# Kernel tuning notes

Measured on AMD Instinct MI355X. Metric: run time of the kernel, lower is better.

## Reference

```python
import jax, jax.numpy as jnp
import numpy as np

N_E = 1024
E_DIM = 64
BETA = 0.25


def setup_inputs() -> dict:
    key = jax.random.key(0)
    k1, k2 = jax.random.split(key)
    z = jax.random.normal(k1, (32, 32, 32, E_DIM), dtype=jnp.float32)
    # torch init: uniform(-1/n_e, 1/n_e)
    codebook = jax.random.uniform(k2, (N_E, E_DIM), dtype=jnp.float32,
                                  minval=-1.0 / N_E, maxval=1.0 / N_E)
    return {"z": z, "codebook": codebook}


def reference(z, codebook):
    z_flat = z.reshape(-1, E_DIM)  # [N, e_dim]
    # squared euclidean distances: ||z||^2 + ||e||^2 - 2 z e^T
    d = (jnp.sum(z_flat ** 2, axis=1, keepdims=True)
         + jnp.sum(codebook ** 2, axis=1)
         - 2.0 * jnp.matmul(z_flat, codebook.T))  # [N, n_e]
    idx = jnp.argmin(d, axis=1)  # [N]
    z_q = codebook[idx].reshape(z.shape)
    sg = jax.lax.stop_gradient
    loss = jnp.mean((sg(z_q) - z) ** 2) + BETA * jnp.mean((z_q - sg(z)) ** 2)
    z_q_st = z + sg(z_q - z)  # straight-through estimator
    return z_q_st, idx, loss
```

## Files before the change

### kernel.cpp

```cpp
#include <hip/hip_runtime.h>

#define NROWS 32768
#define NE    1024
#define ED    64
#define CHUNK 128
#define NCH   (NE / CHUNK)
#define RPW   8

typedef float4 f4;
typedef float2 f2;

__global__ void vq_prep(const float* __restrict__ cb, float* __restrict__ ssq)
{
    int j = blockIdx.x * blockDim.x + threadIdx.x;
    const f4* crow = (const f4*)(cb + (size_t)j * ED);
    float v[ED];
#pragma unroll
    for (int i = 0; i < 16; ++i) {
        f4 t = crow[i];
        v[4*i+0] = t.x; v[4*i+1] = t.y; v[4*i+2] = t.z; v[4*i+3] = t.w;
    }
    {
#pragma clang fp contract(off)
        float r0 = v[0]*v[0], r1 = v[1]*v[1], r2 = v[2]*v[2], r3 = v[3]*v[3];
        float r4 = v[4]*v[4], r5 = v[5]*v[5], r6 = v[6]*v[6], r7 = v[7]*v[7];
#pragma unroll
        for (int i = 8; i < ED; i += 8) {
            r0 += v[i+0]*v[i+0]; r1 += v[i+1]*v[i+1];
            r2 += v[i+2]*v[i+2]; r3 += v[i+3]*v[i+3];
            r4 += v[i+4]*v[i+4]; r5 += v[i+5]*v[i+5];
            r6 += v[i+6]*v[i+6]; r7 += v[i+7]*v[i+7];
        }
        ssq[j] = ((r0+r1)+(r2+r3)) + ((r4+r5)+(r6+r7));
    }
}

__global__ __launch_bounds__(256, 4)
void vq_main(const float* __restrict__ z, const float* __restrict__ cb,
             const float* __restrict__ ssq, float* __restrict__ out,
             float* __restrict__ partials)
{
    __shared__ __align__(16) float et[ED * CHUNK];
    __shared__ __align__(16) float sqsh[NE];
    __shared__ int   idxsh[32];
    __shared__ float wsum[4];

    const int tid  = threadIdx.x;
    const int lane = tid & 63;
    const int w    = tid >> 6;
    const int w_u  = __builtin_amdgcn_readfirstlane(w);
    const int rowbase = blockIdx.x * 32;

    ((f4*)sqsh)[tid] = ((const f4*)ssq)[tid];

    float cn[RPW];
    {
        const int rl = lane >> 3;
        const int jj = lane & 7;
        const float* zr = z + (size_t)(rowbase + w_u * RPW + rl) * ED;
        float a;
        {
#pragma clang fp contract(off)
            a = 0.f;
#pragma unroll
            for (int i = 0; i < 8; ++i) { float v = zr[8*i + jj]; a += v*v; }
        }
        a += __shfl_xor(a, 1);
        a += __shfl_xor(a, 2);
        a += __shfl_xor(a, 4);
#pragma unroll
        for (int r = 0; r < RPW; ++r) cn[r] = __shfl(a, r * 8);
    }

    float bestv[RPW];
    int   besti[RPW];
#pragma unroll
    for (int r = 0; r < RPW; ++r) { bestv[r] = INFINITY; besti[r] = 0; }

    const f2* et2 = (const f2*)et;
    const float* zw = z + (size_t)(rowbase + w_u * RPW) * ED;

    for (int ch = 0; ch < NCH; ++ch) {
        __syncthreads();
        {
            const int c = tid & 127;
            const int h = tid >> 7;
            const f4* crow = (const f4*)(cb + (size_t)(ch * CHUNK + c) * ED
                                         + h * 32);
#pragma unroll
            for (int i = 0; i < 8; ++i) {
                f4 t = crow[i];
                const int dim = h * 32 + 4 * i;
                et[(dim+0) * CHUNK + c] = t.x;
                et[(dim+1) * CHUNK + c] = t.y;
                et[(dim+2) * CHUNK + c] = t.z;
                et[(dim+3) * CHUNK + c] = t.w;
            }
        }
        __syncthreads();

        f2 sv = ((const f2*)sqsh)[ch * 64 + lane];
        float svq[2] = {sv.x, sv.y};

        float acc[RPW][2];
#pragma unroll
        for (int r = 0; r < RPW; ++r) acc[r][0] = acc[r][1] = 0.f;

#pragma unroll 2
        for (int k4 = 0; k4 < 16; ++k4) {
            f2 e0 = et2[(4*k4+0) * 64 + lane];
            f2 e1 = et2[(4*k4+1) * 64 + lane];
            f2 e2 = et2[(4*k4+2) * 64 + lane];
            f2 e3 = et2[(4*k4+3) * 64 + lane];
            f4 z0 = *(const f4*)(zw + 0*ED + 4*k4);
            f4 z1 = *(const f4*)(zw + 1*ED + 4*k4);
            f4 z2 = *(const f4*)(zw + 2*ED + 4*k4);
            f4 z3 = *(const f4*)(zw + 3*ED + 4*k4);
            f4 z4 = *(const f4*)(zw + 4*ED + 4*k4);
            f4 z5 = *(const f4*)(zw + 5*ED + 4*k4);
            f4 z6 = *(const f4*)(zw + 6*ED + 4*k4);
            f4 z7 = *(const f4*)(zw + 7*ED + 4*k4);
#define ROWFMA(r, zz)                                                    \
            acc[r][0] = fmaf(zz.x, e0.x, acc[r][0]);                     \
            acc[r][1] = fmaf(zz.x, e0.y, acc[r][1]);                     \
            acc[r][0] = fmaf(zz.y, e1.x, acc[r][0]);                     \
            acc[r][1] = fmaf(zz.y, e1.y, acc[r][1]);                     \
            acc[r][0] = fmaf(zz.z, e2.x, acc[r][0]);                     \
            acc[r][1] = fmaf(zz.z, e2.y, acc[r][1]);                     \
            acc[r][0] = fmaf(zz.w, e3.x, acc[r][0]);                     \
            acc[r][1] = fmaf(zz.w, e3.y, acc[r][1]);
            ROWFMA(0, z0) ROWFMA(1, z1) ROWFMA(2, z2) ROWFMA(3, z3)
            ROWFMA(4, z4) ROWFMA(5, z5) ROWFMA(6, z6) ROWFMA(7, z7)
#undef ROWFMA
        }

        {
#pragma clang fp contract(off)
#pragma unroll
            for (int r = 0; r < RPW; ++r) {
#pragma unroll
                for (int q = 0; q < 2; ++q) {
                    float t1 = cn[r] + svq[q];
                    float d  = t1 - 2.0f * acc[r][q];
                    int j = ch * CHUNK + lane * 2 + q;
                    if (d < bestv[r]) { bestv[r] = d; besti[r] = j; }
                }
            }
        }
    }

    float lp = 0.f;
#pragma unroll
    for (int r = 0; r < RPW; ++r) {
        float v = bestv[r];
        int   i = besti[r];
#pragma unroll
        for (int m = 1; m < 64; m <<= 1) {
            float ov = __shfl_xor(v, m);
            int   oi = __shfl_xor(i, m);
            if (ov < v || (ov == v && oi < i)) { v = ov; i = oi; }
        }
        i &= (NE - 1);
        const int grow = rowbase + w * RPW + r;
        float zq, zz, diff, st;
        {
#pragma clang fp contract(off)
            zq   = cb[(size_t)i * ED + lane];
            zz   = z [(size_t)grow * ED + lane];
            diff = zq - zz;
            st   = zz + diff;
            lp  += diff * diff;
        }
        out[(size_t)grow * ED + lane] = st;
        if (lane == 0) idxsh[w * RPW + r] = i;
    }

#pragma unroll
    for (int m = 1; m < 64; m <<= 1) lp += __shfl_xor(lp, m);
    if (lane == 0) wsum[w] = lp;
    __syncthreads();

    if (tid < 32) {
        int iv = idxsh[tid] & (NE - 1);
        out[(size_t)NROWS * ED + rowbase + tid] = (float)iv;
    }
    if (tid == 0)
        partials[blockIdx.x] = (wsum[0] + wsum[1]) + (wsum[2] + wsum[3]);
}

__global__ void vq_finalize(const float* __restrict__ partials,
                            float* __restrict__ out)
{
    __shared__ float red[256];
    int t = threadIdx.x;
    float s = (partials[t] + partials[t + 256]) + (partials[t + 512] + partials[t + 768]);
    red[t] = s;
    __syncthreads();
    for (int m = 128; m > 0; m >>= 1) {
        if (t < m) red[t] += red[t + m];
        __syncthreads();
    }
    if (t == 0) {
        float mean = red[0] / (float)((size_t)NROWS * ED);
        out[(size_t)NROWS * ED + NROWS] = mean + 0.25f * mean;
    }
}

extern "C" void kernel_launch(void* const* d_in, const int* in_sizes, int n_in,
                              void* d_out, int out_size, void* d_ws, size_t ws_size,
                              hipStream_t stream)
{
    (void)in_sizes; (void)n_in; (void)out_size; (void)ws_size;
    const float* z  = (const float*)d_in[0];
    const float* cb = (const float*)d_in[1];
    float* out = (float*)d_out;
    float* ssq      = (float*)d_ws;
    float* partials = ssq + NE;

    vq_prep<<<4, 256, 0, stream>>>(cb, ssq);
    vq_main<<<1024, 256, 0, stream>>>(z, cb, ssq, out, partials);
    vq_finalize<<<1, 256, 0, stream>>>(partials, out);
}
```

Before: 74.38 us.

## Pre-interleave codebook in global memory and split codebook across waves per row group

The prep kernel now also writes a dim-quad-major interleaved copy of the codebook to workspace. The main kernel reads codebook entries directly from global/L2 instead of staging transposed chunks through LDS with per-chunk barriers. Each block now handles 16 rows, with two waves splitting the 1024 codes per 8-row group and merging their argmins through shared memory. The grid is doubled, occupancy is raised to 8 blocks per SIMD, and the epilogue is vectorized to float4. This removes LDS transposes and syncs but relies on L2/cache bandwidth for the codebook reads.

```diff
diff --git a/kernel.cpp b/kernel.cpp
--- a/kernel.cpp
+++ b/kernel.cpp
@@ -3,61 +3,61 @@
 #define NROWS 32768
 #define NE    1024
 #define ED    64
-#define CHUNK 128
-#define NCH   (NE / CHUNK)
-#define RPW   8
 
 typedef float4 f4;
-typedef float2 f2;
-
-__global__ void vq_prep(const float* __restrict__ cb, float* __restrict__ ssq)
+
+__global__ void vq_prep(const float* __restrict__ cb, f4* __restrict__ eTi,
+                        float* __restrict__ ssq)
 {
     int j = blockIdx.x * blockDim.x + threadIdx.x;
     const f4* crow = (const f4*)(cb + (size_t)j * ED);
-    float v[ED];
-#pragma unroll
-    for (int i = 0; i < 16; ++i) {
-        f4 t = crow[i];
-        v[4*i+0] = t.x; v[4*i+1] = t.y; v[4*i+2] = t.z; v[4*i+3] = t.w;
-    }
+    f4 v[16];
+#pragma unroll
+    for (int i = 0; i < 16; ++i) v[i] = crow[i];
     {
 #pragma clang fp contract(off)
-        float r0 = v[0]*v[0], r1 = v[1]*v[1], r2 = v[2]*v[2], r3 = v[3]*v[3];
-        float r4 = v[4]*v[4], r5 = v[5]*v[5], r6 = v[6]*v[6], r7 = v[7]*v[7];
-#pragma unroll
-        for (int i = 8; i < ED; i += 8) {
-            r0 += v[i+0]*v[i+0]; r1 += v[i+1]*v[i+1];
-            r2 += v[i+2]*v[i+2]; r3 += v[i+3]*v[i+3];
-            r4 += v[i+4]*v[i+4]; r5 += v[i+5]*v[i+5];
-            r6 += v[i+6]*v[i+6]; r7 += v[i+7]*v[i+7];
+        float r0 = v[0].x*v[0].x, r1 = v[0].y*v[0].y;
+        float r2 = v[0].z*v[0].z, r3 = v[0].w*v[0].w;
+        float r4 = v[1].x*v[1].x, r5 = v[1].y*v[1].y;
+        float r6 = v[1].z*v[1].z, r7 = v[1].w*v[1].w;
+#pragma unroll
+        for (int q = 2; q < 16; q += 2) {
+            r0 += v[q].x*v[q].x;   r1 += v[q].y*v[q].y;
+            r2 += v[q].z*v[q].z;   r3 += v[q].w*v[q].w;
+            r4 += v[q+1].x*v[q+1].x; r5 += v[q+1].y*v[q+1].y;
+            r6 += v[q+1].z*v[q+1].z; r7 += v[q+1].w*v[q+1].w;
         }
         ssq[j] = ((r0+r1)+(r2+r3)) + ((r4+r5)+(r6+r7));
     }
-}
-
-__global__ __launch_bounds__(256, 4)
+#pragma unroll
+    for (int k4 = 0; k4 < 16; ++k4) eTi[(size_t)k4 * NE + j] = v[k4];
+}
+
+__global__ __launch_bounds__(256, 8)
 void vq_main(const float* __restrict__ z, const float* __restrict__ cb,
-             const float* __restrict__ ssq, float* __restrict__ out,
-             float* __restrict__ partials)
-{
-    __shared__ __align__(16) float et[ED * CHUNK];
-    __shared__ __align__(16) float sqsh[NE];
-    __shared__ int   idxsh[32];
-    __shared__ float wsum[4];
+             const f4* __restrict__ eTi, const float* __restrict__ ssq,
+             float* __restrict__ out, float* __restrict__ partials)
+{
+    __shared__ float cvsh[4][8];
+    __shared__ int   cish[4][8];
+    __shared__ int   idxsh[16];
+    __shared__ float redsh[4];
 
     const int tid  = threadIdx.x;
     const int lane = tid & 63;
     const int w    = tid >> 6;
     const int w_u  = __builtin_amdgcn_readfirstlane(w);
-    const int rowbase = blockIdx.x * 32;
-
-    ((f4*)sqsh)[tid] = ((const f4*)ssq)[tid];
-
-    float cn[RPW];
+    const int rg   = w_u >> 1;
+    const int half = w_u & 1;
+    const int rowbase = blockIdx.x * 16;
+
+    const float* zw = z + (size_t)(rowbase + rg * 8) * ED;
+
+    float cn[8];
     {
         const int rl = lane >> 3;
         const int jj = lane & 7;
-        const float* zr = z + (size_t)(rowbase + w_u * RPW + rl) * ED;
+        const float* zr = zw + (size_t)rl * ED;
         float a;
         {
 #pragma clang fp contract(off)
@@ -69,49 +69,26 @@
         a += __shfl_xor(a, 2);
         a += __shfl_xor(a, 4);
 #pragma unroll
-        for (int r = 0; r < RPW; ++r) cn[r] = __shfl(a, r * 8);
-    }
-
-    float bestv[RPW];
-    int   besti[RPW];
-#pragma unroll
-    for (int r = 0; r < RPW; ++r) { bestv[r] = INFINITY; besti[r] = 0; }
-
-    const f2* et2 = (const f2*)et;
-    const float* zw = z + (size_t)(rowbase + w_u * RPW) * ED;
-
-    for (int ch = 0; ch < NCH; ++ch) {
-        __syncthreads();
-        {
-            const int c = tid & 127;
-            const int h = tid >> 7;
-            const f4* crow = (const f4*)(cb + (size_t)(ch * CHUNK + c) * ED
-                                         + h * 32);
-#pragma unroll
-            for (int i = 0; i < 8; ++i) {
-                f4 t = crow[i];
-                const int dim = h * 32 + 4 * i;
-                et[(dim+0) * CHUNK + c] = t.x;
-                et[(dim+1) * CHUNK + c] = t.y;
-                et[(dim+2) * CHUNK + c] = t.z;
-                et[(dim+3) * CHUNK + c] = t.w;
-            }
-        }
-        __syncthreads();
-
-        f2 sv = ((const f2*)sqsh)[ch * 64 + lane];
-        float svq[2] = {sv.x, sv.y};
-
-        float acc[RPW][2];
-#pragma unroll
-        for (int r = 0; r < RPW; ++r) acc[r][0] = acc[r][1] = 0.f;
-
-#pragma unroll 2
+        for (int r = 0; r < 8; ++r) cn[r] = __shfl(a, r * 8);
+    }
+
+    float bestv[8];
+    int   besti[8];
+#pragma unroll
+    for (int r = 0; r < 8; ++r) { bestv[r] = INFINITY; besti[r] = 0; }
+
+    for (int g = 0; g < 8; ++g) {
+        const int cb0 = half * 512 + g * 64;
+        const int c   = cb0 + lane;
+        const float sq = ssq[c];
+
+        float acc[8];
+#pragma unroll
+        for (int r = 0; r < 8; ++r) acc[r] = 0.f;
+
+#pragma unroll 4
         for (int k4 = 0; k4 < 16; ++k4) {
-            f2 e0 = et2[(4*k4+0) * 64 + lane];
-            f2 e1 = et2[(4*k4+1) * 64 + lane];
-            f2 e2 = et2[(4*k4+2) * 64 + lane];
-            f2 e3 = et2[(4*k4+3) * 64 + lane];
+            f4 e  = eTi[(size_t)k4 * NE + c];
             f4 z0 = *(const f4*)(zw + 0*ED + 4*k4);
             f4 z1 = *(const f4*)(zw + 1*ED + 4*k4);
             f4 z2 = *(const f4*)(zw + 2*ED + 4*k4);
@@ -120,15 +97,11 @@
             f4 z5 = *(const f4*)(zw + 5*ED + 4*k4);
             f4 z6 = *(const f4*)(zw + 6*ED + 4*k4);
             f4 z7 = *(const f4*)(zw + 7*ED + 4*k4);
-#define ROWFMA(r, zz)                                                    \
-            acc[r][0] = fmaf(zz.x, e0.x, acc[r][0]);                     \
-            acc[r][1] = fmaf(zz.x, e0.y, acc[r][1]);                     \
-            acc[r][0] = fmaf(zz.y, e1.x, acc[r][0]);                     \
-            acc[r][1] = fmaf(zz.y, e1.y, acc[r][1]);                     \
-            acc[r][0] = fmaf(zz.z, e2.x, acc[r][0]);                     \
-            acc[r][1] = fmaf(zz.z, e2.y, acc[r][1]);                     \
-            acc[r][0] = fmaf(zz.w, e3.x, acc[r][0]);                     \
-            acc[r][1] = fmaf(zz.w, e3.y, acc[r][1]);
+#define ROWFMA(r, zz)                                 \
+            acc[r] = fmaf(e.x, zz.x, acc[r]);         \
+            acc[r] = fmaf(e.y, zz.y, acc[r]);         \
+            acc[r] = fmaf(e.z, zz.z, acc[r]);         \
+            acc[r] = fmaf(e.w, zz.w, acc[r]);
             ROWFMA(0, z0) ROWFMA(1, z1) ROWFMA(2, z2) ROWFMA(3, z3)
             ROWFMA(4, z4) ROWFMA(5, z5) ROWFMA(6, z6) ROWFMA(7, z7)
 #undef ROWFMA
@@ -137,21 +110,16 @@
         {
 #pragma clang fp contract(off)
 #pragma unroll
-            for (int r = 0; r < RPW; ++r) {
-#pragma unroll
-                for (int q = 0; q < 2; ++q) {
-                    float t1 = cn[r] + svq[q];
-                    float d  = t1 - 2.0f * acc[r][q];
-                    int j = ch * CHUNK + lane * 2 + q;
-                    if (d < bestv[r]) { bestv[r] = d; besti[r] = j; }
-                }
+            for (int r = 0; r < 8; ++r) {
+                float t1 = cn[r] + sq;
+                float d  = t1 - 2.0f * acc[r];
+                if (d < bestv[r]) { bestv[r] = d; besti[r] = c; }
             }
         }
     }
 
-    float lp = 0.f;
-#pragma unroll
-    for (int r = 0; r < RPW; ++r) {
+#pragma unroll
+    for (int r = 0; r < 8; ++r) {
         float v = bestv[r];
         int   i = besti[r];
 #pragma unroll
@@ -160,32 +128,45 @@
             int   oi = __shfl_xor(i, m);
             if (ov < v || (ov == v && oi < i)) { v = ov; i = oi; }
         }
-        i &= (NE - 1);
-        const int grow = rowbase + w * RPW + r;
-        float zq, zz, diff, st;
-        {
-#pragma clang fp contract(off)
-            zq   = cb[(size_t)i * ED + lane];
-            zz   = z [(size_t)grow * ED + lane];
-            diff = zq - zz;
-            st   = zz + diff;
-            lp  += diff * diff;
-        }
-        out[(size_t)grow * ED + lane] = st;
-        if (lane == 0) idxsh[w * RPW + r] = i;
-    }
+        if (lane == 0) { cvsh[w][r] = v; cish[w][r] = i; }
+    }
+    __syncthreads();
+
+    if (tid < 16) {
+        const int r  = tid & 7;
+        const int g2 = tid >> 3;
+        float v0 = cvsh[g2*2][r];   int i0 = cish[g2*2][r];
+        float v1 = cvsh[g2*2+1][r]; int i1 = cish[g2*2+1][r];
+        int ii = (v1 < v0 || (v1 == v0 && i1 < i0)) ? i1 : i0;
+        ii &= (NE - 1);
+        idxsh[tid] = ii;
+        out[(size_t)NROWS * ED + rowbase + tid] = (float)ii;
+    }
+    __syncthreads();
+
+    const int erow = tid >> 4;
+    const int q4   = tid & 15;
+    const int gi   = idxsh[erow];
+    f4 e  = *(const f4*)(cb + (size_t)gi * ED + q4 * 4);
+    f4 zz = *(const f4*)(z + (size_t)(rowbase + erow) * ED + q4 * 4);
+    float lp;
+    f4 o;
+    {
+#pragma clang fp contract(off)
+        float d0 = e.x - zz.x; o.x = zz.x + d0;
+        float d1 = e.y - zz.y; o.y = zz.y + d1;
+        float d2 = e.z - zz.z; o.z = zz.z + d2;
+        float d3 = e.w - zz.w; o.w = zz.w + d3;
+        lp = ((d0*d0 + d1*d1) + (d2*d2 + d3*d3));
+    }
+    *(f4*)(out + (size_t)(rowbase + erow) * ED + q4 * 4) = o;
 
 #pragma unroll
     for (int m = 1; m < 64; m <<= 1) lp += __shfl_xor(lp, m);
-    if (lane == 0) wsum[w] = lp;
-    __syncthreads();
-
-    if (tid < 32) {
-        int iv = idxsh[tid] & (NE - 1);
-        out[(size_t)NROWS * ED + rowbase + tid] = (float)iv;
-    }
+    if (lane == 0) redsh[w] = lp;
+    __syncthreads();
     if (tid == 0)
-        partials[blockIdx.x] = (wsum[0] + wsum[1]) + (wsum[2] + wsum[3]);
+        partials[blockIdx.x] = (redsh[0] + redsh[1]) + (redsh[2] + redsh[3]);
 }
 
 __global__ void vq_finalize(const float* __restrict__ partials,
@@ -193,8 +174,11 @@
 {
     __shared__ float red[256];
     int t = threadIdx.x;
-    float s = (partials[t] + partials[t + 256]) + (partials[t + 512] + partials[t + 768]);
-    red[t] = s;
+    float a = (partials[t]        + partials[t + 256])
+            + (partials[t + 512]  + partials[t + 768]);
+    float b = (partials[t + 1024] + partials[t + 1280])
+            + (partials[t + 1536] + partials[t + 1792]);
+    red[t] = a + b;
     __syncthreads();
     for (int m = 128; m > 0; m >>= 1) {
         if (t < m) red[t] += red[t + m];
@@ -214,10 +198,12 @@
     const float* z  = (const float*)d_in[0];
     const float* cb = (const float*)d_in[1];
     float* out = (float*)d_out;
-    float* ssq      = (float*)d_ws;
+
+    f4*    eTi      = (f4*)d_ws;
+    float* ssq      = (float*)d_ws + 16 * NE * 4;
     float* partials = ssq + NE;
 
-    vq_prep<<<4, 256, 0, stream>>>(cb, ssq);
-    vq_main<<<1024, 256, 0, stream>>>(z, cb, ssq, out, partials);
+    vq_prep<<<4, 256, 0, stream>>>(cb, eTi, ssq);
+    vq_main<<<2048, 256, 0, stream>>>(z, cb, eTi, ssq, out, partials);
     vq_finalize<<<1, 256, 0, stream>>>(partials, out);
 }
```

Result: slower. 250.1 us (+236.3%).
